# Kernel optimization log

Hardware: AMD Instinct MI355X
Metric: run time of the kernel (lower is better)

## Reference

```python
import jax, jax.numpy as jnp
import numpy as np
import math

N, IN, OUT, E, K = 50000, 256, 256, 800000, 32

def setup_inputs() -> dict:
    key = jax.random.key(0)
    k0, k1, k2, k3, k4 = jax.random.split(key, 5)
    feat = jax.random.normal(k0, (N, IN), dtype=jnp.float32)
    # xavier_uniform with relu gain, as in reset_parameters
    gain = math.sqrt(2.0)
    a = gain * math.sqrt(6.0 / (IN + OUT))
    W_self = jax.random.uniform(k1, (OUT, IN), minval=-a, maxval=a, dtype=jnp.float32)
    W_neigh = jax.random.uniform(k2, (OUT, IN), minval=-a, maxval=a, dtype=jnp.float32)
    b_neigh = jnp.zeros((OUT,), dtype=jnp.float32)
    # random CSR graph: E edges, row pointers from sorted cut points
    indices = jax.random.randint(k3, (E,), 0, N, dtype=jnp.int32)
    inner = jnp.sort(jax.random.randint(k4, (N - 1,), 0, E, dtype=jnp.int32))
    indptr = jnp.concatenate([jnp.zeros((1,), jnp.int32), inner,
                              jnp.full((1,), E, jnp.int32)])
    return {"feat": feat, "W_self": W_self, "W_neigh": W_neigh,
            "b_neigh": b_neigh, "indices": indices, "indptr": indptr}

def reference(feat, W_self, W_neigh, b_neigh, indices, indptr):
    n = feat.shape[0]
    # feat_drop with p=0.0 is identity
    h_self = feat @ W_self.T                      # [N, OUT]
    feat_neigh = feat @ W_neigh.T + b_neigh       # [N, OUT]
    # MaxK: keep top-k entries per row, zero the rest
    vals, idx = jax.lax.top_k(feat_neigh, K)      # [N, K]
    rows = jnp.arange(n)[:, None]
    masked = jnp.zeros_like(feat_neigh).at[rows, idx].set(vals)
    # CSR SpMM with unit values (sum over neighbors)
    deg = indptr[1:] - indptr[:-1]                # [N]
    dst = jnp.repeat(jnp.arange(n, dtype=jnp.int32), deg,
                     total_repeat_length=indices.shape[0])
    h_neigh = jax.ops.segment_sum(masked[indices], dst, num_segments=n)
    return h_self + h_neigh
```

## Files before the change

### kernel.cpp

```cpp
#include <hip/hip_runtime.h>

#define N_NODES 50000
#define TOPK 32
#define SOFT_DELTA 2e-5f

typedef unsigned long long u64;
typedef unsigned u32;
typedef float f32x16 __attribute__((ext_vector_type(16)));
typedef __bf16 bf16x8 __attribute__((ext_vector_type(8)));

__device__ __forceinline__ float dec(u32 u) {
    return __builtin_bit_cast(float, (u & 0x80000000u) ? (u & 0x7FFFFFFFu) : ~u);
}
__device__ __forceinline__ int mbcnt64(u64 m) {
    return __builtin_amdgcn_mbcnt_hi((u32)(m >> 32),
           __builtin_amdgcn_mbcnt_lo((u32)m, 0u));
}

__device__ __forceinline__ void gll16(const uint4* g, uint4* l) {
    __builtin_amdgcn_global_load_lds(
        (const __attribute__((address_space(1))) void*)g,
        (__attribute__((address_space(3))) void*)l, 16, 0, 0);
}

__device__ __forceinline__ u32 enc4(float v, int col) {
    return ((u32)col << 16) |
           ((__builtin_bit_cast(u32, v) + 0x8000u) >> 16);
}

__device__ __forceinline__ u32 s2(float x0, float x1, float& r0, float& r1) {
    const u32 h0 = (__builtin_bit_cast(u32, x0) + 0x8000u) & 0xFFFF0000u;
    const u32 h1 = (__builtin_bit_cast(u32, x1) + 0x8000u) & 0xFFFF0000u;
    r0 = x0 - __builtin_bit_cast(float, h0);
    r1 = x1 - __builtin_bit_cast(float, h1);
    return (h0 >> 16) | h1;
}
__device__ __forceinline__ u32 p2(float x0, float x1) {
    return (((__builtin_bit_cast(u32, x0) + 0x8000u) & 0xFFFF0000u) >> 16) |
           ((__builtin_bit_cast(u32, x1) + 0x8000u) & 0xFFFF0000u);
}

struct Tri { uint4 h1, h2, h3; };
__device__ __forceinline__ Tri cvt8(const float4 u, const float4 v, bool deep) {
    Tri t;
    float r0,r1,r2,r3,r4,r5,r6,r7;
    t.h1.x = s2(u.x, u.y, r0, r1);
    t.h1.y = s2(u.z, u.w, r2, r3);
    t.h1.z = s2(v.x, v.y, r4, r5);
    t.h1.w = s2(v.z, v.w, r6, r7);
    float s0,s1,s2_,s3,s4,s5,s6,s7;
    t.h2.x = s2(r0, r1, s0, s1);
    t.h2.y = s2(r2, r3, s2_, s3);
    t.h2.z = s2(r4, r5, s4, s5);
    t.h2.w = s2(r6, r7, s6, s7);
    if (deep) {
        t.h3.x = p2(s0, s1); t.h3.y = p2(s2_, s3);
        t.h3.z = p2(s4, s5); t.h3.w = p2(s6, s7);
    } else {
        t.h3 = make_uint4(0, 0, 0, 0);
    }
    return t;
}

__global__ __launch_bounds__(256) void wprep_kernel(
    const float* __restrict__ Wself, const float* __restrict__ Wneigh,
    uint4* __restrict__ WTn1, uint4* __restrict__ WTn2,
    uint4* __restrict__ WTn3, uint4* __restrict__ WTs1)
{
    for (int it = 0; it < 4; ++it) {
        const int id = (blockIdx.x * 4 + it) * 256 + threadIdx.x;
        const int s = id >> 10, rem = id & 1023;
        const int c = rem >> 8, j = rem & 255;
        const float* srcN = Wneigh + (size_t)j * 256 + s * 32 + c * 8;
        const Tri tn = cvt8(*(const float4*)srcN, *(const float4*)(srcN + 4), true);
        WTn1[id] = tn.h1; WTn2[id] = tn.h2; WTn3[id] = tn.h3;
        const float* srcS = Wself + (size_t)j * 256 + s * 32 + c * 8;
        const Tri ts = cvt8(*(const float4*)srcS, *(const float4*)(srcS + 4), false);
        WTs1[id] = ts.h1;
    }
}

__global__ __launch_bounds__(512, 4) void gemm_all_kernel(
    const float* __restrict__ feat,
    const uint4* __restrict__ WTn1, const uint4* __restrict__ WTn2,
    const uint4* __restrict__ WTn3, const uint4* __restrict__ WTs1,
    const float* __restrict__ bneigh,
    float* __restrict__ hself,
    u32*  __restrict__ compact,
    u64*  __restrict__ softList)
{
    __shared__ uint4 SMEM[4864];
    uint4* LA1  = SMEM;
    uint4* LA2  = SMEM + 256;
    uint4* LA3  = SMEM + 512;
    uint4* LBn1 = SMEM + 768;
    uint4* LBn2 = SMEM + 1792;
    uint4* LBn3 = SMEM + 2816;
    uint4* LBs1 = SMEM + 3840;
    float* stage = (float*)SMEM;

    const int tid  = threadIdx.x;
    const int lane = tid & 63;
    const int wave = tid >> 6;
    const int kg   = lane >> 5;

    const int row0 = blockIdx.x * 64;

    const int ar = tid & 63;
    const int ac = (tid >> 6) & 3;
    int gra = row0 + ar;
    if (gra >= N_NODES) gra = row0;
    const float* pa = feat + (size_t)gra * 256 + ac * 8;
    const int aidx = ac * 64 + ar;

    const int rA0  = lane & 31;
    const int bcol = wave * 32 + (lane & 31);

    f32x16 accN[2], accS[2];
    accN[0] = (f32x16)0.f; accN[1] = (f32x16)0.f;
    accS[0] = (f32x16)0.f; accS[1] = (f32x16)0.f;

    float4 va0 = make_float4(0,0,0,0), va1 = make_float4(0,0,0,0);
    if (tid < 256) { va0 = *(const float4*)(pa); va1 = *(const float4*)(pa + 4); }

    for (int s = 0; s < 8; ++s) {
        __syncthreads();
        {
            const int base = s * 1024;
            const int w64  = wave * 64;
            gll16(WTn1 + base + w64 + lane,       LBn1 + w64);
            gll16(WTn1 + base + 512 + w64 + lane, LBn1 + 512 + w64);
            gll16(WTn2 + base + w64 + lane,       LBn2 + w64);
            gll16(WTn2 + base + 512 + w64 + lane, LBn2 + 512 + w64);
            gll16(WTn3 + base + w64 + lane,       LBn3 + w64);
            gll16(WTn3 + base + 512 + w64 + lane, LBn3 + 512 + w64);
            gll16(WTs1 + base + w64 + lane,       LBs1 + w64);
            gll16(WTs1 + base + 512 + w64 + lane, LBs1 + 512 + w64);
        }
        if (tid < 256) {
            const Tri t = cvt8(va0, va1, true);
            LA1[aidx] = t.h1; LA2[aidx] = t.h2; LA3[aidx] = t.h3;
            if (s < 7) {
                const int ko = (s + 1) * 32;
                va0 = *(const float4*)(pa + ko);
                va1 = *(const float4*)(pa + ko + 4);
            }
        }
        __syncthreads();

#pragma unroll
        for (int ks = 0; ks < 2; ++ks) {
            const int ch = (ks << 1) | kg;
            bf16x8 a1[2], a2[2], a3[2], b1, b2, b3, bs;
            {
                const int ib = ch * 256 + bcol;
                b1 = __builtin_bit_cast(bf16x8, LBn1[ib]);
                b2 = __builtin_bit_cast(bf16x8, LBn2[ib]);
                b3 = __builtin_bit_cast(bf16x8, LBn3[ib]);
                bs = __builtin_bit_cast(bf16x8, LBs1[ib]);
            }
#pragma unroll
            for (int f = 0; f < 2; ++f) {
                const int ia = ch * 64 + rA0 + f * 32;
                a1[f] = __builtin_bit_cast(bf16x8, LA1[ia]);
                a2[f] = __builtin_bit_cast(bf16x8, LA2[ia]);
                a3[f] = __builtin_bit_cast(bf16x8, LA3[ia]);
            }
#pragma unroll
            for (int i = 0; i < 2; ++i) {
                accN[i] = __builtin_amdgcn_mfma_f32_32x32x16_bf16(a1[i], b1, accN[i], 0, 0, 0);
                accN[i] = __builtin_amdgcn_mfma_f32_32x32x16_bf16(a1[i], b2, accN[i], 0, 0, 0);
                accN[i] = __builtin_amdgcn_mfma_f32_32x32x16_bf16(a2[i], b1, accN[i], 0, 0, 0);
                accN[i] = __builtin_amdgcn_mfma_f32_32x32x16_bf16(a2[i], b2, accN[i], 0, 0, 0);
                accN[i] = __builtin_amdgcn_mfma_f32_32x32x16_bf16(a1[i], b3, accN[i], 0, 0, 0);
                accN[i] = __builtin_amdgcn_mfma_f32_32x32x16_bf16(a3[i], b1, accN[i], 0, 0, 0);
                accS[i] = __builtin_amdgcn_mfma_f32_32x32x16_bf16(a1[i], bs, accS[i], 0, 0, 0);
                accS[i] = __builtin_amdgcn_mfma_f32_32x32x16_bf16(a2[i], bs, accS[i], 0, 0, 0);
            }
        }
    }

#pragma unroll
    for (int i = 0; i < 2; ++i) {
        const int rbase = i * 32 + (kg << 2);
#pragma unroll
        for (int r = 0; r < 16; ++r) {
            const int grow = row0 + rbase + (r & 3) + ((r >> 2) << 3);
            if (grow < N_NODES)
                hself[(size_t)grow * 256 + bcol] = accS[i][r];
        }
    }

    __syncthreads();
    const float bn = bneigh[bcol];
#pragma unroll
    for (int i = 0; i < 2; ++i) {
        const int rbase = i * 32 + (kg << 2);
#pragma unroll
        for (int r = 0; r < 16; ++r) {
            const int rl = rbase + (r & 3) + ((r >> 2) << 3);
            stage[rl * 256 + bcol] = accN[i][r] + bn;
        }
    }
    __syncthreads();

    for (int it = 0; it < 8; ++it) {
        const int rl  = wave * 8 + it;
        const int row = row0 + rl;
        if (row >= N_NODES) break;

        const float4 v4 = ((const float4*)stage)[rl * 64 + lane];
        const float vv[4] = {v4.x, v4.y, v4.z, v4.w};
        u32 key[4];
#pragma unroll
        for (int j = 0; j < 4; ++j) {
            const u32 b = __builtin_bit_cast(u32, vv[j]);
            key[j] = (b & 0x80000000u) ? ~b : (b | 0x80000000u);
        }

        u32 T = 0;
        bool resolved = false;
        for (int b = 31; b >= 0; --b) {
            const u32 t2 = T | (1u << b);
            int cnt = 0;
#pragma unroll
            for (int j = 0; j < 4; ++j) cnt += __popcll(__ballot(key[j] >= t2));
            if (cnt >= TOPK) T = t2;
            if (cnt == TOPK) { resolved = true; break; }
        }
        if (resolved) {
            u32 x = 0xFFFFFFFFu;
#pragma unroll
            for (int j = 0; j < 4; ++j)
                x = min(x, (key[j] >= T) ? key[j] : 0xFFFFFFFFu);
#pragma unroll
            for (int off = 32; off >= 1; off >>= 1)
                x = min(x, (u32)__shfl_xor((int)x, off, 64));
            T = x;
        }

        u64 bgt[4], beq[4];
        int cgt = 0, ceq = 0;
#pragma unroll
        for (int j = 0; j < 4; ++j) {
            bgt[j] = __ballot(key[j] > T);
            beq[j] = __ballot(key[j] == T);
            cgt += __popcll(bgt[j]);
            ceq += __popcll(beq[j]);
        }
        const int r_ = TOPK - cgt;

        u32 m33;
        if (ceq > r_) {
            m33 = T;
        } else {
            u32 x = 0;
#pragma unroll
            for (int j = 0; j < 4; ++j) x = max(x, (key[j] < T) ? key[j] : 0u);
#pragma unroll
            for (int off = 32; off >= 1; off >>= 1)
                x = max(x, (u32)__shfl_xor((int)x, off, 64));
            m33 = x;
        }
        const float v32f = dec(T);
        const float v33f = dec(m33);
        const bool soft = (v32f - v33f) < SOFT_DELTA;

        const int meqsum = mbcnt64(beq[0]) + mbcnt64(beq[1]) +
                           mbcnt64(beq[2]) + mbcnt64(beq[3]);

        int gtbase = 0, selfpre = 0, spillcol = -1;
#pragma unroll
        for (int j = 0; j < 4; ++j) {
            const int col = lane * 4 + j;
            if (key[j] > T) {
                const int pos = gtbase + mbcnt64(bgt[j]);
                compact[(size_t)row * 32 + pos] = enc4(vv[j], col);
            } else if (key[j] == T) {
                const int eqrank = meqsum + selfpre;
                if (eqrank < r_) {
                    const float w = (soft && eqrank == r_ - 1) ? 0.5f : 1.0f;
                    compact[(size_t)row * 32 + (cgt + eqrank)] = enc4(vv[j] * w, col);
                } else if (eqrank == r_) {
                    spillcol = col;
                }
                ++selfpre;
            }
            gtbase += __popcll(bgt[j]);
        }

        if (soft) {
            const u64 valbits = (u64)__builtin_bit_cast(u32, 0.5f * v33f);
            if (ceq > r_) {
                if (spillcol >= 0)
                    softList[row] = (((u64)(u32)spillcol) << 32) | valbits;
            } else {
                int best = 1 << 30;
#pragma unroll
                for (int j = 0; j < 4; ++j) {
                    const u64 b33 = __ballot(key[j] == m33);
                    if (b33) best = min(best, ((int)__builtin_ctzll(b33)) * 4 + j);
                }
                if (lane == 0)
                    softList[row] = (((u64)(u32)best) << 32) | valbits;
            }
        } else if (lane == 0) {
            softList[row] = 0ull;
        }
    }
}

__global__ __launch_bounds__(512) void spmm_kernel(
    const u32* __restrict__ compact,
    const u64* __restrict__ softList,
    const int* __restrict__ indices,
    const int* __restrict__ indptr,
    float* __restrict__ inout)
{
    __shared__ float accs[8][2][256];

    const int lane = threadIdx.x & 63;
    const int wave = threadIdx.x >> 6;
    const int node = blockIdx.x * 8 + wave;
    const int half = lane >> 5;
    const int e    = lane & 31;
    float* acc  = accs[wave][half];

    const float4 z4 = make_float4(0.f, 0.f, 0.f, 0.f);
    ((float4*)&accs[wave][0][0])[lane] = z4;
    ((float4*)&accs[wave][1][0])[lane] = z4;

    const int start = indptr[node];
    const int deg   = indptr[node + 1] - start;
    const float4 hs = ((const float4*)(inout + (size_t)node * 256))[lane];

    for (int base = 0; base < deg; base += 64) {
        const int n = min(64, deg - base);
        const int myidx = (base + lane < deg) ? indices[start + base + lane] : 0;
        for (int d = 0; d < n; d += 16) {
            int s[8]; bool ok[8]; u32 ent[8];
#pragma unroll
            for (int k = 0; k < 8; ++k) {
                const int ei = d + 2 * k + half;
                ok[k] = ei < n;
                s[k]  = __shfl(myidx, min(ei, n - 1), 64);
                ent[k] = compact[(size_t)s[k] * 32 + e];
            }
            u64 se[8];
            if (e == 0) {
#pragma unroll
                for (int k = 0; k < 8; ++k) se[k] = softList[s[k]];
            }
#pragma unroll
            for (int k = 0; k < 8; ++k) {
                const int c = (int)(ent[k] >> 16);
                float v = __builtin_bit_cast(float, ent[k] << 16);
                if (!ok[k]) v = 0.f;
                acc[c] += v;
                if (e == 0 && ok[k]) {
                    const u32 vb = (u32)se[k];
                    if (vb)
                        acc[(int)(se[k] >> 32)] += __builtin_bit_cast(float, vb);
                }
            }
        }
    }

    const float4 a0 = ((const float4*)&accs[wave][0][0])[lane];
    const float4 a1 = ((const float4*)&accs[wave][1][0])[lane];
    float4 o;
    o.x = a0.x + a1.x + hs.x;
    o.y = a0.y + a1.y + hs.y;
    o.z = a0.z + a1.z + hs.z;
    o.w = a0.w + a1.w + hs.w;
    ((float4*)(inout + (size_t)node * 256))[lane] = o;
}

extern "C" void kernel_launch(void* const* d_in, const int* in_sizes, int n_in,
                              void* d_out, int out_size, void* d_ws, size_t ws_size,
                              hipStream_t stream) {
    const float* feat   = (const float*)d_in[0];
    const float* Wself  = (const float*)d_in[1];
    const float* Wneigh = (const float*)d_in[2];
    const float* bneigh = (const float*)d_in[3];
    const int* indices  = (const int*)d_in[4];
    const int* indptr   = (const int*)d_in[5];
    float* out = (float*)d_out;

    char* ws       = (char*)d_ws;
    u32*  compact  = (u32*)(ws);
    u64*  softList = (u64*)(ws + 6400000);
    uint4* WTn1    = (uint4*)(ws + 6800000);
    uint4* WTn2    = WTn1 + 8192;
    uint4* WTn3    = WTn2 + 8192;
    uint4* WTs1    = WTn3 + 8192;

    wprep_kernel<<<dim3(8), dim3(256), 0, stream>>>(
        Wself, Wneigh, WTn1, WTn2, WTn3, WTs1);

    const int rowTiles64 = (N_NODES + 63) / 64;
    gemm_all_kernel<<<dim3(rowTiles64), dim3(512), 0, stream>>>(
        feat, WTn1, WTn2, WTn3, WTs1, bneigh, out, compact, softList);

    const int spmmBlocks = N_NODES / 8;
    spmm_kernel<<<dim3(spmmBlocks), dim3(512), 0, stream>>>(
        compact, softList, indices, indptr, out);
}
```

Baseline: 262.9 us.

## Halve GEMM row tile to 32 rows with 16-wide K steps and smaller LDS

Shrinks the fused GEMM+top-k block from 64 to 32 rows and splits K into 16 steps of 16 instead of 8 steps of 32. This cuts LDS per block and doubles the grid size so more blocks can be resident and the load is spread more evenly. The cost is that each weight tile is reused across half as many rows, so weight traffic from L2 doubles, and there are twice as many barrier-separated K iterations. Launch bounds are relaxed from 4 to 3 blocks per CU.

```diff
diff --git a/kernel.cpp b/kernel.cpp
--- a/kernel.cpp
+++ b/kernel.cpp
@@ -80,7 +80,7 @@
     }
 }
 
-__global__ __launch_bounds__(512, 4) void gemm_all_kernel(
+__global__ __launch_bounds__(512, 3) void gemm_all_kernel(
     const float* __restrict__ feat,
     const uint4* __restrict__ WTn1, const uint4* __restrict__ WTn2,
     const uint4* __restrict__ WTn3, const uint4* __restrict__ WTs1,
@@ -89,14 +89,14 @@
     u32*  __restrict__ compact,
     u64*  __restrict__ softList)
 {
-    __shared__ uint4 SMEM[4864];
-    uint4* LA1  = SMEM;
-    uint4* LA2  = SMEM + 256;
-    uint4* LA3  = SMEM + 512;
-    uint4* LBn1 = SMEM + 768;
-    uint4* LBn2 = SMEM + 1792;
-    uint4* LBn3 = SMEM + 2816;
-    uint4* LBs1 = SMEM + 3840;
+    __shared__ uint4 SMEM[2304];
+    uint4* LBn1 = SMEM;
+    uint4* LBn2 = SMEM + 512;
+    uint4* LBn3 = SMEM + 1024;
+    uint4* LBs1 = SMEM + 1536;
+    uint4* LA1  = SMEM + 2048;
+    uint4* LA2  = SMEM + 2112;
+    uint4* LA3  = SMEM + 2176;
     float* stage = (float*)SMEM;
 
     const int tid  = threadIdx.x;
@@ -104,108 +104,79 @@
     const int wave = tid >> 6;
     const int kg   = lane >> 5;
 
-    const int row0 = blockIdx.x * 64;
-
-    const int ar = tid & 63;
-    const int ac = (tid >> 6) & 3;
+    const int row0 = blockIdx.x * 32;
+
+    const int ar  = tid >> 3;
+    const int akp = tid & 7;
     int gra = row0 + ar;
     if (gra >= N_NODES) gra = row0;
-    const float* pa = feat + (size_t)gra * 256 + ac * 8;
-    const int aidx = ac * 64 + ar;
+    const float* pa = feat + (size_t)gra * 256 + akp * 2;
+    const int widx = ((akp >> 2) << 7) + (ar << 2) + (akp & 3);
 
     const int rA0  = lane & 31;
     const int bcol = wave * 32 + (lane & 31);
 
-    f32x16 accN[2], accS[2];
-    accN[0] = (f32x16)0.f; accN[1] = (f32x16)0.f;
-    accS[0] = (f32x16)0.f; accS[1] = (f32x16)0.f;
-
-    float4 va0 = make_float4(0,0,0,0), va1 = make_float4(0,0,0,0);
-    if (tid < 256) { va0 = *(const float4*)(pa); va1 = *(const float4*)(pa + 4); }
-
-    for (int s = 0; s < 8; ++s) {
+    f32x16 accN = (f32x16)0.f, accS = (f32x16)0.f;
+
+    float2 va = make_float2(0.f, 0.f);
+    if (tid < 256) va = *(const float2*)(pa);
+
+    for (int s = 0; s < 16; ++s) {
         __syncthreads();
         {
-            const int base = s * 1024;
-            const int w64  = wave * 64;
-            gll16(WTn1 + base + w64 + lane,       LBn1 + w64);
-            gll16(WTn1 + base + 512 + w64 + lane, LBn1 + 512 + w64);
-            gll16(WTn2 + base + w64 + lane,       LBn2 + w64);
-            gll16(WTn2 + base + 512 + w64 + lane, LBn2 + 512 + w64);
-            gll16(WTn3 + base + w64 + lane,       LBn3 + w64);
-            gll16(WTn3 + base + 512 + w64 + lane, LBn3 + 512 + w64);
-            gll16(WTs1 + base + w64 + lane,       LBs1 + w64);
-            gll16(WTs1 + base + 512 + w64 + lane, LBs1 + 512 + w64);
+            const int bsrc = (s >> 1) * 1024 + (s & 1) * 512 + (wave << 6) + lane;
+            const int bdst = wave << 6;
+            gll16(WTn1 + bsrc, LBn1 + bdst);
+            gll16(WTn2 + bsrc, LBn2 + bdst);
+            gll16(WTn3 + bsrc, LBn3 + bdst);
+            gll16(WTs1 + bsrc, LBs1 + bdst);
         }
         if (tid < 256) {
-            const Tri t = cvt8(va0, va1, true);
-            LA1[aidx] = t.h1; LA2[aidx] = t.h2; LA3[aidx] = t.h3;
-            if (s < 7) {
-                const int ko = (s + 1) * 32;
-                va0 = *(const float4*)(pa + ko);
-                va1 = *(const float4*)(pa + ko + 4);
-            }
+            float r0, r1, q0, q1;
+            const u32 h1 = s2(va.x, va.y, r0, r1);
+            const u32 h2 = s2(r0, r1, q0, q1);
+            const u32 h3 = p2(q0, q1);
+            ((u32*)LA1)[widx] = h1;
+            ((u32*)LA2)[widx] = h2;
+            ((u32*)LA3)[widx] = h3;
+            if (s < 15) va = *(const float2*)(pa + (s + 1) * 16);
         }
         __syncthreads();
 
-#pragma unroll
-        for (int ks = 0; ks < 2; ++ks) {
-            const int ch = (ks << 1) | kg;
-            bf16x8 a1[2], a2[2], a3[2], b1, b2, b3, bs;
-            {
-                const int ib = ch * 256 + bcol;
-                b1 = __builtin_bit_cast(bf16x8, LBn1[ib]);
-                b2 = __builtin_bit_cast(bf16x8, LBn2[ib]);
-                b3 = __builtin_bit_cast(bf16x8, LBn3[ib]);
-                bs = __builtin_bit_cast(bf16x8, LBs1[ib]);
-            }
-#pragma unroll
-            for (int f = 0; f < 2; ++f) {
-                const int ia = ch * 64 + rA0 + f * 32;
-                a1[f] = __builtin_bit_cast(bf16x8, LA1[ia]);
-                a2[f] = __builtin_bit_cast(bf16x8, LA2[ia]);
-                a3[f] = __builtin_bit_cast(bf16x8, LA3[ia]);
-            }
-#pragma unroll
-            for (int i = 0; i < 2; ++i) {
-                accN[i] = __builtin_amdgcn_mfma_f32_32x32x16_bf16(a1[i], b1, accN[i], 0, 0, 0);
-                accN[i] = __builtin_amdgcn_mfma_f32_32x32x16_bf16(a1[i], b2, accN[i], 0, 0, 0);
-                accN[i] = __builtin_amdgcn_mfma_f32_32x32x16_bf16(a2[i], b1, accN[i], 0, 0, 0);
-                accN[i] = __builtin_amdgcn_mfma_f32_32x32x16_bf16(a2[i], b2, accN[i], 0, 0, 0);
-                accN[i] = __builtin_amdgcn_mfma_f32_32x32x16_bf16(a1[i], b3, accN[i], 0, 0, 0);
-                accN[i] = __builtin_amdgcn_mfma_f32_32x32x16_bf16(a3[i], b1, accN[i], 0, 0, 0);
-                accS[i] = __builtin_amdgcn_mfma_f32_32x32x16_bf16(a1[i], bs, accS[i], 0, 0, 0);
-                accS[i] = __builtin_amdgcn_mfma_f32_32x32x16_bf16(a2[i], bs, accS[i], 0, 0, 0);
-            }
-        }
-    }
-
-#pragma unroll
-    for (int i = 0; i < 2; ++i) {
-        const int rbase = i * 32 + (kg << 2);
-#pragma unroll
-        for (int r = 0; r < 16; ++r) {
-            const int grow = row0 + rbase + (r & 3) + ((r >> 2) << 3);
-            if (grow < N_NODES)
-                hself[(size_t)grow * 256 + bcol] = accS[i][r];
-        }
+        const int ia = (kg << 5) + rA0;
+        const int ib = (kg << 8) + bcol;
+        const bf16x8 a1 = __builtin_bit_cast(bf16x8, LA1[ia]);
+        const bf16x8 a2 = __builtin_bit_cast(bf16x8, LA2[ia]);
+        const bf16x8 a3 = __builtin_bit_cast(bf16x8, LA3[ia]);
+        const bf16x8 b1 = __builtin_bit_cast(bf16x8, LBn1[ib]);
+        const bf16x8 b2 = __builtin_bit_cast(bf16x8, LBn2[ib]);
+        const bf16x8 b3 = __builtin_bit_cast(bf16x8, LBn3[ib]);
+        const bf16x8 bs = __builtin_bit_cast(bf16x8, LBs1[ib]);
+
+        accN = __builtin_amdgcn_mfma_f32_32x32x16_bf16(a1, b1, accN, 0, 0, 0);
+        accN = __builtin_amdgcn_mfma_f32_32x32x16_bf16(a1, b2, accN, 0, 0, 0);
+        accN = __builtin_amdgcn_mfma_f32_32x32x16_bf16(a2, b1, accN, 0, 0, 0);
+        accN = __builtin_amdgcn_mfma_f32_32x32x16_bf16(a2, b2, accN, 0, 0, 0);
+        accN = __builtin_amdgcn_mfma_f32_32x32x16_bf16(a1, b3, accN, 0, 0, 0);
+        accN = __builtin_amdgcn_mfma_f32_32x32x16_bf16(a3, b1, accN, 0, 0, 0);
+        accS = __builtin_amdgcn_mfma_f32_32x32x16_bf16(a1, bs, accS, 0, 0, 0);
+        accS = __builtin_amdgcn_mfma_f32_32x32x16_bf16(a2, bs, accS, 0, 0, 0);
     }
 
     __syncthreads();
     const float bn = bneigh[bcol];
 #pragma unroll
-    for (int i = 0; i < 2; ++i) {
-        const int rbase = i * 32 + (kg << 2);
-#pragma unroll
-        for (int r = 0; r < 16; ++r) {
-            const int rl = rbase + (r & 3) + ((r >> 2) << 3);
-            stage[rl * 256 + bcol] = accN[i][r] + bn;
-        }
+    for (int r = 0; r < 16; ++r) {
+        const int rl = (kg << 2) + (r & 3) + ((r >> 2) << 3);
+        stage[rl * 256 + bcol] = accN[r] + bn;
+        const int grow = row0 + rl;
+        if (grow < N_NODES)
+            hself[(size_t)grow * 256 + bcol] = accS[r];
     }
     __syncthreads();
 
-    for (int it = 0; it < 8; ++it) {
-        const int rl  = wave * 8 + it;
+    for (int it = 0; it < 4; ++it) {
+        const int rl  = wave * 4 + it;
         const int row = row0 + rl;
         if (row >= N_NODES) break;
 
@@ -398,8 +369,8 @@
     wprep_kernel<<<dim3(8), dim3(256), 0, stream>>>(
         Wself, Wneigh, WTn1, WTn2, WTn3, WTs1);
 
-    const int rowTiles64 = (N_NODES + 63) / 64;
-    gemm_all_kernel<<<dim3(rowTiles64), dim3(512), 0, stream>>>(
+    const int rowTiles32 = (N_NODES + 31) / 32;
+    gemm_all_kernel<<<dim3(rowTiles32), dim3(512), 0, stream>>>(
         feat, WTn1, WTn2, WTn3, WTs1, bneigh, out, compact, softList);
 
     const int spmmBlocks = N_NODES / 8;
```

Result: faster. 250.7 us, median of 2 (-4.6%).
